# Kernel optimization log

Hardware: AMD Instinct MI355X
Metric: run time of the kernel (lower is better)

The kernel has to match this reference:

```python
import jax, jax.numpy as jnp
import numpy as np

EPS = 1e-5
K = 5

def _bn(x, g, b):
    # BatchNorm1d in training mode: biased batch statistics
    mu = jnp.mean(x, axis=0)
    var = jnp.mean((x - mu) ** 2, axis=0)
    return (x - mu) * jax.lax.rsqrt(var + EPS) * g + b

def setup_inputs():
    key = jax.random.key(0)
    ks = jax.random.split(key, 16)
    N, M, D, F = 16384, 8192, 512, 2048
    s = 0.02
    return dict(
        src=jax.random.normal(ks[0], (N, D), jnp.float32),
        anchor_2=jax.random.normal(ks[1], (M, D), jnp.float32),
        W_dim=jax.random.normal(ks[2], (D, D), jnp.float32) * s,
        b_dim=jnp.zeros((D,), jnp.float32),
        W_fus=jax.random.normal(ks[3], (2 * D, D), jnp.float32) * s,
        b_fus=jnp.zeros((D,), jnp.float32),
        W_e1=jax.random.normal(ks[4], (D, F), jnp.float32) * s,
        b_e1=jnp.zeros((F,), jnp.float32),
        W_e2=jax.random.normal(ks[5], (F, D), jnp.float32) * s,
        b_e2=jnp.zeros((D,), jnp.float32),
        g1=jnp.ones((D,), jnp.float32), bt1=jnp.zeros((D,), jnp.float32),
        g2=jnp.ones((D,), jnp.float32), bt2=jnp.zeros((D,), jnp.float32),
        W_d=jax.random.normal(ks[6], (D, D), jnp.float32) * s,
        b_d=jnp.zeros((D,), jnp.float32),
        g_d=jnp.ones((D,), jnp.float32), bt_d=jnp.zeros((D,), jnp.float32),
    )

def reference(src, anchor_2, W_dim, b_dim, W_fus, b_fus, W_e1, b_e1, W_e2, b_e2,
              g1, bt1, g2, bt2, W_d, b_d, g_d, bt_d):
    # kNN in Euclidean metric (sklearn NearestNeighbors): squared distances suffice
    # d2[n,m] = ||src_n||^2 - 2 src_n . a_m + ||a_m||^2   -> [N, M]
    d2 = (jnp.sum(src * src, axis=1, keepdims=True)
          - 2.0 * (src @ anchor_2.T)
          + jnp.sum(anchor_2 * anchor_2, axis=1)[None, :])
    _, idx = jax.lax.top_k(-d2, K)                      # [N, K] nearest anchors
    neigh = jnp.mean(anchor_2[idx], axis=1)             # gather + mean -> [N, D]
    a_map = neigh @ W_dim + b_dim                       # linear_dim
    comb = jnp.concatenate([src, a_map], axis=1) @ W_fus + b_fus
    comb = _bn(comb, g1, bt1)                           # norm1
    # encoder MLP (dropout is identity in eval)
    t = jnp.tanh(comb @ W_e1 + b_e1) @ W_e2 + b_e2
    comb = _bn(comb + t, g2, bt2)                       # residual + norm2
    out = jnp.tanh(_bn(comb @ W_d + b_d, g_d, bt_d))    # decoder
    return out
```

## Files before the change

kernel.cpp:

```cpp
#include <hip/hip_runtime.h>
#include <math.h>

#define N_ROWS 16384
#define M_ANCH 8192
#define DDIM   512
#define FDIM   2048
#define KNN    5
#define BN_EPS 1e-5f
#define CHUNK  8192
#define SEED   1024
#define CAND_MAX 256
#define MARGIN 6.0f
#define QSCALE 28.0f
#define TWO_INV_S2 (2.0f / (QSCALE * QSCALE))

typedef _Float16 f16;
typedef _Float16 f16x8 __attribute__((ext_vector_type(8)));
typedef _Float16 f16x4 __attribute__((ext_vector_type(4)));
typedef float f32x4 __attribute__((ext_vector_type(4)));
typedef int   i32x4 __attribute__((ext_vector_type(4)));

__device__ __forceinline__ void async_copy16(const void* g, void* l) {
    __builtin_amdgcn_global_load_lds(
        (const __attribute__((address_space(1))) void*)g,
        (__attribute__((address_space(3))) void*)l, 16, 0, 0);
}

__device__ __forceinline__ bool kless(float k1, int i1, float k2, int i2) {
    return (k1 < k2) || (k1 == k2 && i1 < i2);
}

__device__ __forceinline__ void insert5(float (&bk)[KNN], int (&bi)[KNN], float key, int id) {
    if (!kless(key, id, bk[4], bi[4])) return;
    bool c3 = kless(key, id, bk[3], bi[3]);
    bool c2 = kless(key, id, bk[2], bi[2]);
    bool c1 = kless(key, id, bk[1], bi[1]);
    bool c0 = kless(key, id, bk[0], bi[0]);
    bk[4] = c3 ? bk[3] : key;                  bi[4] = c3 ? bi[3] : id;
    bk[3] = c3 ? (c2 ? bk[2] : key) : bk[3];   bi[3] = c3 ? (c2 ? bi[2] : id) : bi[3];
    bk[2] = c2 ? (c1 ? bk[1] : key) : bk[2];   bi[2] = c2 ? (c1 ? bi[1] : id) : bi[2];
    bk[1] = c1 ? (c0 ? bk[0] : key) : bk[1];   bi[1] = c1 ? (c0 ? bi[0] : id) : bi[1];
    bk[0] = c0 ? key : bk[0];                  bi[0] = c0 ? id : bi[0];
}

__global__ void zero_kernel(float* p, int n) {
    int i = blockIdx.x * blockDim.x + threadIdx.x;
    if (i < n) p[i] = 0.f;
}

__global__ __launch_bounds__(256) void quant_i8_kernel(const float* __restrict__ X,
                                                       unsigned int* __restrict__ Y, int n4) {
    int i = blockIdx.x * 256 + threadIdx.x;
    if (i >= n4) return;
    float4 v = ((const float4*)X)[i];
    int a = (int)rintf(v.x * QSCALE); a = a > 127 ? 127 : (a < -127 ? -127 : a);
    int b = (int)rintf(v.y * QSCALE); b = b > 127 ? 127 : (b < -127 ? -127 : b);
    int c = (int)rintf(v.z * QSCALE); c = c > 127 ? 127 : (c < -127 ? -127 : c);
    int d = (int)rintf(v.w * QSCALE); d = d > 127 ? 127 : (d < -127 ? -127 : d);
    Y[i] = (unsigned int)(a & 255) | ((unsigned int)(b & 255) << 8)
         | ((unsigned int)(c & 255) << 16) | ((unsigned int)(d & 255) << 24);
}

__global__ __launch_bounds__(256) void rowsplit_kernel(const float* __restrict__ X,
                                                       f16* __restrict__ Y,
                                                       int n4, int log_k4) {
    int i4 = blockIdx.x * 256 + threadIdx.x;
    if (i4 >= n4) return;
    int K4 = 1 << log_k4;
    int row = i4 >> log_k4;
    int kc = (i4 & (K4 - 1)) * 4;
    float4 v = ((const float4*)X)[i4];
    f16x4 h, lo;
    h.x = (f16)v.x; h.y = (f16)v.y; h.z = (f16)v.z; h.w = (f16)v.w;
    lo.x = (f16)(v.x - (float)h.x); lo.y = (f16)(v.y - (float)h.y);
    lo.z = (f16)(v.z - (float)h.z); lo.w = (f16)(v.w - (float)h.w);
    f16* base = Y + (size_t)row * (K4 * 8) + kc;
    *(f16x4*)base = h;
    *(f16x4*)(base + K4 * 4) = lo;
}

__global__ __launch_bounds__(256) void anchor_norm_kernel(const float* __restrict__ a,
                                                          float* __restrict__ norm_a) {
    int wave = threadIdx.x >> 6, lane = threadIdx.x & 63;
    int row = blockIdx.x * 4 + wave;
    const float4* ar = (const float4*)(a + (size_t)row * DDIM);
    float4 v1 = ar[lane * 2];
    float4 v2 = ar[lane * 2 + 1];
    float s = v1.x*v1.x + v1.y*v1.y + v1.z*v1.z + v1.w*v1.w
            + v2.x*v2.x + v2.y*v2.y + v2.z*v2.z + v2.w*v2.w;
    for (int off = 32; off; off >>= 1) s += __shfl_xor(s, off, 64);
    if (lane == 0) norm_a[row] = s;
}

template<int COLLECT>
__global__ __launch_bounds__(256) void gemm_i8(
    const char* __restrict__ A, const char* __restrict__ B,
    const float* __restrict__ norm, const float* __restrict__ thr,
    int* __restrict__ cnt, int* __restrict__ cand_i, float* __restrict__ cand_n,
    int idofs, float* __restrict__ C, int Ncols)
{
    __shared__ char As[2][128 * 64];
    __shared__ char Bs[2][128 * 64];
    const int t = threadIdx.x;
    const int w = t >> 6, l = t & 63;
    const int m0 = blockIdx.y * 128, n0 = blockIdx.x * 128;
    const int wm = (w & 1) * 64, wn = (w >> 1) * 64;

    i32x4 acc[4][4];
    #pragma unroll
    for (int i = 0; i < 4; ++i)
        #pragma unroll
        for (int j = 0; j < 4; ++j) acc[i][j] = (i32x4){0, 0, 0, 0};

    const int srow = l >> 2;
    const int gq = ((l & 3) - (srow >> 1)) & 3;
    const int skoff = gq * 16;
    const int sqf = (((l >> 4) + (((l & 15) >> 1) & 3)) & 3) * 16;

    auto STAGE = [&](int buf, int kt) {
        int k0 = kt * 64;
        #pragma unroll
        for (int s = 0; s < 2; ++s) {
            int grp = w * 2 + s;
            int row = grp * 16 + srow;
            async_copy16(A + (size_t)(m0 + row) * DDIM + k0 + skoff,
                         &As[buf][grp * 1024 + l * 16]);
            async_copy16(B + (size_t)(n0 + row) * DDIM + k0 + skoff,
                         &Bs[buf][grp * 1024 + l * 16]);
        }
    };

    STAGE(0, 0);
    __syncthreads();

    for (int kt = 0; kt < 8; ++kt) {
        int cur = kt & 1;
        if (kt < 7) STAGE(cur ^ 1, kt + 1);
        i32x4 af[4], bf[4];
        #pragma unroll
        for (int i = 0; i < 4; ++i)
            af[i] = *(const i32x4*)&As[cur][(wm + i * 16 + (l & 15)) * 64 + sqf];
        #pragma unroll
        for (int j = 0; j < 4; ++j)
            bf[j] = *(const i32x4*)&Bs[cur][(wn + j * 16 + (l & 15)) * 64 + sqf];
        #pragma unroll
        for (int i = 0; i < 4; ++i)
            #pragma unroll
            for (int j = 0; j < 4; ++j)
                acc[i][j] = __builtin_amdgcn_mfma_i32_16x16x64_i8(af[i], bf[j], acc[i][j], 0, 0, 0);
        __syncthreads();
    }

    float nj[4];
    #pragma unroll
    for (int j = 0; j < 4; ++j) nj[j] = norm[n0 + wn + j * 16 + (l & 15)];

    if (COLLECT) {
        float thr4[4][4];
        #pragma unroll
        for (int i = 0; i < 4; ++i) {
            float4 tv = *(const float4*)&thr[m0 + wm + i * 16 + (l >> 4) * 4];
            thr4[i][0] = tv.x; thr4[i][1] = tv.y; thr4[i][2] = tv.z; thr4[i][3] = tv.w;
        }
        #pragma unroll
        for (int i = 0; i < 4; ++i)
            #pragma unroll
            for (int j = 0; j < 4; ++j)
                #pragma unroll
                for (int r = 0; r < 4; ++r) {
                    float key = nj[j] - TWO_INV_S2 * (float)acc[i][j][r];
                    if (key < thr4[i][r]) {
                        int row = m0 + wm + i * 16 + (l >> 4) * 4 + r;
                        int pos = atomicAdd(&cnt[row], 1);
                        if (pos < CAND_MAX) {
                            cand_i[(size_t)row * CAND_MAX + pos] =
                                idofs + n0 + wn + j * 16 + (l & 15);
                            cand_n[(size_t)row * CAND_MAX + pos] = nj[j];
                        }
                    }
                }
    } else {
        #pragma unroll
        for (int i = 0; i < 4; ++i)
            #pragma unroll
            for (int j = 0; j < 4; ++j)
                #pragma unroll
                for (int r = 0; r < 4; ++r) {
                    int m = m0 + wm + i * 16 + (l >> 4) * 4 + r;
                    int n = n0 + wn + j * 16 + (l & 15);
                    C[(size_t)m * Ncols + n] = nj[j] - TWO_INV_S2 * (float)acc[i][j][r];
                }
    }
}

__global__ __launch_bounds__(256) void topk_scan_kernel(
    const float* __restrict__ g, const float* __restrict__ norm_a,
    float* __restrict__ thrbuf, int* __restrict__ cnt,
    int* __restrict__ cand_i, float* __restrict__ cand_n)
{
    int row = blockIdx.x * 4 + (threadIdx.x >> 6);
    int lane = threadIdx.x & 63;
    const float* grow = g + (size_t)row * SEED;
    float4 v0 = *(const float4*)(grow + lane * 4);
    float4 v1 = *(const float4*)(grow + 256 + lane * 4);
    float4 v2 = *(const float4*)(grow + 512 + lane * 4);
    float4 v3 = *(const float4*)(grow + 768 + lane * 4);
    float bk[KNN]; int bi[KNN];
    #pragma unroll
    for (int q = 0; q < KNN; ++q) { bk[q] = 3.0e38f; bi[q] = 0x7fffffff; }
    int c = lane * 4;
    insert5(bk, bi, v0.x, c);       insert5(bk, bi, v0.y, c + 1);
    insert5(bk, bi, v0.z, c + 2);   insert5(bk, bi, v0.w, c + 3);
    insert5(bk, bi, v1.x, c + 256); insert5(bk, bi, v1.y, c + 257);
    insert5(bk, bi, v1.z, c + 258); insert5(bk, bi, v1.w, c + 259);
    insert5(bk, bi, v2.x, c + 512); insert5(bk, bi, v2.y, c + 513);
    insert5(bk, bi, v2.z, c + 514); insert5(bk, bi, v2.w, c + 515);
    insert5(bk, bi, v3.x, c + 768); insert5(bk, bi, v3.y, c + 769);
    insert5(bk, bi, v3.z, c + 770); insert5(bk, bi, v3.w, c + 771);
    for (int off = 32; off >= 1; off >>= 1) {
        float ok[KNN]; int oi[KNN];
        #pragma unroll
        for (int q = 0; q < KNN; ++q) {
            ok[q] = __shfl_xor(bk[q], off, 64);
            oi[q] = __shfl_xor(bi[q], off, 64);
        }
        #pragma unroll
        for (int q = 0; q < KNN; ++q) insert5(bk, bi, ok[q], oi[q]);
    }
    float thr = bk[4] + MARGIN;
    if (lane == 0) thrbuf[row] = thr;
    int* rci = cand_i + (size_t)row * CAND_MAX;
    float* rcn = cand_n + (size_t)row * CAND_MAX;
    #define PUSH(v, id) if ((v) < thr) { int pos = atomicAdd(&cnt[row], 1); \
                                         if (pos < CAND_MAX) { rci[pos] = (id); \
                                         rcn[pos] = norm_a[(id)]; } }
    PUSH(v0.x, c)       PUSH(v0.y, c + 1)   PUSH(v0.z, c + 2)   PUSH(v0.w, c + 3)
    PUSH(v1.x, c + 256) PUSH(v1.y, c + 257) PUSH(v1.z, c + 258) PUSH(v1.w, c + 259)
    PUSH(v2.x, c + 512) PUSH(v2.y, c + 513) PUSH(v2.z, c + 514) PUSH(v2.w, c + 515)
    PUSH(v3.x, c + 768) PUSH(v3.y, c + 769) PUSH(v3.z, c + 770) PUSH(v3.w, c + 771)
    #undef PUSH
}

__global__ __launch_bounds__(256) void rescore_kernel(
    const float* __restrict__ src, const float* __restrict__ anchor,
    const int* __restrict__ cnt, const int* __restrict__ cand_i,
    const float* __restrict__ cand_n, float* __restrict__ neigh)
{
    __shared__ float lb[4][2][DDIM];
    int wv = threadIdx.x >> 6, lane = threadIdx.x & 63;
    int row = blockIdx.x * 4 + wv;
    const float4* sp = (const float4*)(src + (size_t)row * DDIM);
    float4 s0 = sp[lane * 2], s1 = sp[lane * 2 + 1];
    int c = cnt[row]; if (c > CAND_MAX) c = CAND_MAX;
    const int* ci = cand_i + (size_t)row * CAND_MAX;
    const float* cn = cand_n + (size_t)row * CAND_MAX;

    float bk[KNN]; int bi[KNN];
    #pragma unroll
    for (int q = 0; q < KNN; ++q) { bk[q] = 3.0e38f; bi[q] = 0x7fffffff; }

    auto PREF = [&](int buf, int id) {
        const float* gp = anchor + (size_t)id * DDIM;
        async_copy16(gp + lane * 8,     &lb[wv][buf][lane * 4]);
        async_copy16(gp + lane * 8 + 4, &lb[wv][buf][256 + lane * 4]);
    };

    int   id_c = ci[0];          float n_c = cn[0];
    int   id_n = ci[1];          float n_n = cn[1];
    PREF(0, id_c);
    PREF(1, id_n);

    for (int p = 0; p < c; ++p) {
        int id_f = 0; float n_f = 0.f;
        if (p + 2 < c) { id_f = ci[p + 2]; n_f = cn[p + 2]; }
        asm volatile("s_waitcnt vmcnt(4)" ::: "memory");
        const float* bc = &lb[wv][p & 1][0];
        float4 a0 = *(const float4*)&bc[lane * 4];
        float4 a1 = *(const float4*)&bc[256 + lane * 4];
        float d = s0.x*a0.x + s0.y*a0.y + s0.z*a0.z + s0.w*a0.w
                + s1.x*a1.x + s1.y*a1.y + s1.z*a1.z + s1.w*a1.w;
        #pragma unroll
        for (int off = 32; off; off >>= 1) d += __shfl_xor(d, off, 64);
        insert5(bk, bi, n_c - 2.f * d, id_c);
        if (p + 2 < c) PREF(p & 1, id_f);
        id_c = id_n; n_c = n_n;
        id_n = id_f; n_n = n_f;
    }

    const float4* a0 = (const float4*)(anchor + (size_t)bi[0] * DDIM);
    const float4* a1 = (const float4*)(anchor + (size_t)bi[1] * DDIM);
    const float4* a2 = (const float4*)(anchor + (size_t)bi[2] * DDIM);
    const float4* a3 = (const float4*)(anchor + (size_t)bi[3] * DDIM);
    const float4* a4 = (const float4*)(anchor + (size_t)bi[4] * DDIM);
    float4* np = (float4*)(neigh + (size_t)row * DDIM);
    #pragma unroll
    for (int p = 0; p < 2; ++p) {
        int c4 = lane + 64 * p;
        float4 v0 = a0[c4], v1 = a1[c4], v2 = a2[c4], v3 = a3[c4], v4 = a4[c4];
        float4 o;
        o.x = (v0.x + v1.x + v2.x + v3.x + v4.x) * 0.2f;
        o.y = (v0.y + v1.y + v2.y + v3.y + v4.y) * 0.2f;
        o.z = (v0.z + v1.z + v2.z + v3.z + v4.z) * 0.2f;
        o.w = (v0.w + v1.w + v2.w + v3.w + v4.w) * 0.2f;
        np[c4] = o;
    }
}

template<int ADDC0, int TANH, int K>
__global__ __launch_bounds__(256) void gemm_f16hl(
    const f16* __restrict__ Aw, const f16* __restrict__ Bw,
    const float* __restrict__ bias, const float* __restrict__ C0,
    float* __restrict__ C, int Ncols)
{
    __shared__ f16 Ah[2][128 * 32];
    __shared__ f16 Al[2][128 * 32];
    __shared__ f16 Bh[2][128 * 32];
    __shared__ f16 Bl[2][128 * 32];
    const int t = threadIdx.x;
    const int w = t >> 6, l = t & 63;
    const int m0 = blockIdx.y * 128, n0 = blockIdx.x * 128;
    const int wm = (w & 1) * 64, wn = (w >> 1) * 64;
    const int K2 = 2 * K;
    const int NK = K / 32;

    f32x4 acc[4][4];
    #pragma unroll
    for (int i = 0; i < 4; ++i)
        #pragma unroll
        for (int j = 0; j < 4; ++j) acc[i][j] = (f32x4){0.f, 0.f, 0.f, 0.f};

    const int srow = l >> 2;
    const int gq = ((l & 3) - (srow >> 1)) & 3;
    const int skoff = gq * 8;
    const int sqf = (((l >> 4) + (((l & 15) >> 1) & 3)) & 3) * 8;

    auto STAGE = [&](int buf, int kt) {
        int k0 = kt * 32;
        #pragma unroll
        for (int s = 0; s < 2; ++s) {
            int grp = w * 2 + s;
            int row = grp * 16 + srow;
            const f16* ap = Aw + (size_t)(m0 + row) * K2 + k0 + skoff;
            async_copy16(ap,     &Ah[buf][grp * 512 + l * 8]);
            async_copy16(ap + K, &Al[buf][grp * 512 + l * 8]);
            const f16* bp = Bw + (size_t)(n0 + row) * K2 + k0 + skoff;
            async_copy16(bp,     &Bh[buf][grp * 512 + l * 8]);
            async_copy16(bp + K, &Bl[buf][grp * 512 + l * 8]);
        }
    };

    STAGE(0, 0);
    __syncthreads();

    for (int kt = 0; kt < NK; ++kt) {
        int cur = kt & 1;
        if (kt + 1 < NK) STAGE(cur ^ 1, kt + 1);
        f16x8 afh[4], afl[4], bfh[4], bfl[4];
        #pragma unroll
        for (int i = 0; i < 4; ++i) {
            int base = (wm + i * 16 + (l & 15)) * 32 + sqf;
            afh[i] = *(const f16x8*)&Ah[cur][base];
            afl[i] = *(const f16x8*)&Al[cur][base];
        }
        #pragma unroll
        for (int j = 0; j < 4; ++j) {
            int base = (wn + j * 16 + (l & 15)) * 32 + sqf;
            bfh[j] = *(const f16x8*)&Bh[cur][base];
            bfl[j] = *(const f16x8*)&Bl[cur][base];
        }
        #pragma unroll
        for (int i = 0; i < 4; ++i)
            #pragma unroll
            for (int j = 0; j < 4; ++j) {
                acc[i][j] = __builtin_amdgcn_mfma_f32_16x16x32_f16(afh[i], bfh[j], acc[i][j], 0, 0, 0);
                acc[i][j] = __builtin_amdgcn_mfma_f32_16x16x32_f16(afl[i], bfh[j], acc[i][j], 0, 0, 0);
                acc[i][j] = __builtin_amdgcn_mfma_f32_16x16x32_f16(afh[i], bfl[j], acc[i][j], 0, 0, 0);
            }
        __syncthreads();
    }
    float bv[4];
    #pragma unroll
    for (int j = 0; j < 4; ++j)
        bv[j] = bias ? bias[n0 + wn + j * 16 + (l & 15)] : 0.f;
    #pragma unroll
    for (int i = 0; i < 4; ++i)
        #pragma unroll
        for (int j = 0; j < 4; ++j)
            #pragma unroll
            for (int r = 0; r < 4; ++r) {
                int m = m0 + wm + i * 16 + (l >> 4) * 4 + r;
                int n = n0 + wn + j * 16 + (l & 15);
                float v = acc[i][j][r] + bv[j];
                if (ADDC0) v += C0[(size_t)m * Ncols + n];
                if (TANH)  v = tanhf(v);
                C[(size_t)m * Ncols + n] = v;
            }
}

__global__ __launch_bounds__(256) void wsplit_kernel(const float* __restrict__ W,
                                                     f16* __restrict__ Wt,
                                                     int K, int N)
{
    __shared__ float tile[64][65];
    const int t = threadIdx.x;
    const int kb = blockIdx.y * 64, nb = blockIdx.x * 64;
    #pragma unroll
    for (int i = 0; i < 4; ++i) {
        int r = (t >> 4) + i * 16;
        int c = (t & 15) * 4;
        *(float4*)&tile[r][c] = *(const float4*)&W[(size_t)(kb + r) * N + nb + c];
    }
    __syncthreads();
    const int r2 = t >> 2;
    const int kc = (t & 3) * 16;
    f16x8 h0, h1, lo0, lo1;
    #pragma unroll
    for (int e = 0; e < 8; ++e) {
        float x = tile[kc + e][r2];
        f16 hh = (f16)x; h0[e] = hh; lo0[e] = (f16)(x - (float)hh);
        float y = tile[kc + 8 + e][r2];
        f16 hh2 = (f16)y; h1[e] = hh2; lo1[e] = (f16)(y - (float)hh2);
    }
    f16* base = Wt + (size_t)(nb + r2) * 2 * K + kb + kc;
    *(f16x8*)base = h0; *(f16x8*)(base + 8) = h1;
    *(f16x8*)(base + K) = lo0; *(f16x8*)(base + K + 8) = lo1;
}

__global__ __launch_bounds__(256) void bcomb_kernel(const float* __restrict__ b_dim,
                                                    const float* __restrict__ W_fus2,
                                                    const float* __restrict__ b_fus,
                                                    float* __restrict__ b_comb)
{
    int n = blockIdx.x * 256 + threadIdx.x;
    if (n >= DDIM) return;
    float s = b_fus[n];
    for (int k = 0; k < DDIM; ++k) s += b_dim[k] * W_fus2[(size_t)k * DDIM + n];
    b_comb[n] = s;
}

template<int ACT>
__global__ __launch_bounds__(256) void gemm_kernel(
    const float* __restrict__ A, int K1,
    const float* __restrict__ A2, int K2,
    const float* __restrict__ B, const float* __restrict__ bias,
    float* __restrict__ C, int Ncols)
{
    __shared__ float As[16][132];
    __shared__ float Bs[16][128];
    const int t = threadIdx.x;
    const int n0 = blockIdx.x * 128;
    const int m0 = blockIdx.y * 128;
    const int ty = t >> 4, tx = t & 15;
    const int K = K1 + K2;

    float acc[8][8];
    #pragma unroll
    for (int i = 0; i < 8; ++i)
        #pragma unroll
        for (int j = 0; j < 8; ++j) acc[i][j] = 0.f;

    const int ar = t >> 1;
    const int akc = (t & 1) * 8;
    const int bkr = t >> 4;
    const int bc = (t & 15) * 8;

    for (int k0 = 0; k0 < K; k0 += 16) {
        int kk = k0 + akc;
        float4 v0, v1;
        if (kk < K1) {
            const float* p = A + (size_t)(m0 + ar) * K1 + kk;
            v0 = *(const float4*)p; v1 = *(const float4*)(p + 4);
        } else {
            const float* p = A2 + (size_t)(m0 + ar) * K2 + (kk - K1);
            v0 = *(const float4*)p; v1 = *(const float4*)(p + 4);
        }
        const float* bp = B + (size_t)(k0 + bkr) * Ncols + n0 + bc;
        float4 w0 = *(const float4*)bp, w1 = *(const float4*)(bp + 4);
        __syncthreads();
        As[akc+0][ar] = v0.x; As[akc+1][ar] = v0.y; As[akc+2][ar] = v0.z; As[akc+3][ar] = v0.w;
        As[akc+4][ar] = v1.x; As[akc+5][ar] = v1.y; As[akc+6][ar] = v1.z; As[akc+7][ar] = v1.w;
        *(float4*)&Bs[bkr][bc] = w0; *(float4*)&Bs[bkr][bc + 4] = w1;
        __syncthreads();
        #pragma unroll
        for (int k = 0; k < 16; ++k) {
            float a[8], b[8];
            *(float4*)&a[0] = *(const float4*)&As[k][ty * 8];
            *(float4*)&a[4] = *(const float4*)&As[k][ty * 8 + 4];
            *(float4*)&b[0] = *(const float4*)&Bs[k][tx * 4];
            *(float4*)&b[4] = *(const float4*)&Bs[k][64 + tx * 4];
            #pragma unroll
            for (int i = 0; i < 8; ++i)
                #pragma unroll
                for (int j = 0; j < 8; ++j) acc[i][j] += a[i] * b[j];
        }
    }
    float4 bv0 = *(const float4*)(bias + n0 + tx * 4);
    float4 bv1 = *(const float4*)(bias + n0 + 64 + tx * 4);
    #pragma unroll
    for (int i = 0; i < 8; ++i) {
        int row = m0 + ty * 8 + i;
        float4 o0, o1;
        o0.x = acc[i][0] + bv0.x; o0.y = acc[i][1] + bv0.y;
        o0.z = acc[i][2] + bv0.z; o0.w = acc[i][3] + bv0.w;
        o1.x = acc[i][4] + bv1.x; o1.y = acc[i][5] + bv1.y;
        o1.z = acc[i][6] + bv1.z; o1.w = acc[i][7] + bv1.w;
        if (ACT == 1) {
            o0.x = tanhf(o0.x); o0.y = tanhf(o0.y); o0.z = tanhf(o0.z); o0.w = tanhf(o0.w);
            o1.x = tanhf(o1.x); o1.y = tanhf(o1.y); o1.z = tanhf(o1.z); o1.w = tanhf(o1.w);
        }
        *(float4*)(C + (size_t)row * Ncols + n0 + tx * 4) = o0;
        *(float4*)(C + (size_t)row * Ncols + n0 + 64 + tx * 4) = o1;
    }
}

__global__ __launch_bounds__(256) void bn_stats_kernel(const float* __restrict__ X,
                                                       float* __restrict__ sums)
{
    __shared__ float red[8][64];
    int lane = threadIdx.x & 63;
    int rl = threadIdx.x >> 6;
    int c = blockIdx.x * 64 + lane;
    int chunk = N_ROWS / gridDim.y;
    int rbeg = blockIdx.y * chunk;
    float s = 0.f, s2 = 0.f;
    for (int r = rbeg + rl; r < rbeg + chunk; r += 4) {
        float v = X[(size_t)r * DDIM + c];
        s += v; s2 += v * v;
    }
    red[rl][lane] = s; red[4 + rl][lane] = s2;
    __syncthreads();
    if (threadIdx.x < 64) {
        float ts = red[0][lane] + red[1][lane] + red[2][lane] + red[3][lane];
        float t2 = red[4][lane] + red[5][lane] + red[6][lane] + red[7][lane];
        atomicAdd(&sums[c], ts);
        atomicAdd(&sums[DDIM + c], t2);
    }
}

template<int TANH>
__global__ __launch_bounds__(256) void bn_apply_kernel(
    const float* __restrict__ X, float* __restrict__ Y,
    const float* __restrict__ sums, const float* __restrict__ g,
    const float* __restrict__ b, float invN)
{
    size_t i = (size_t)blockIdx.x * 256 + threadIdx.x;
    int cg = (int)(i % (DDIM / 4));
    int c = cg * 4;
    float4 x = ((const float4*)X)[i];
    float4 sm = *(const float4*)(sums + c);
    float4 sq = *(const float4*)(sums + DDIM + c);
    float4 gv = *(const float4*)(g + c);
    float4 bv = *(const float4*)(b + c);
    float m, var, rs;
    m = sm.x * invN; var = sq.x * invN - m * m; rs = rsqrtf(var + BN_EPS);
    x.x = (x.x - m) * rs * gv.x + bv.x;
    m = sm.y * invN; var = sq.y * invN - m * m; rs = rsqrtf(var + BN_EPS);
    x.y = (x.y - m) * rs * gv.y + bv.y;
    m = sm.z * invN; var = sq.z * invN - m * m; rs = rsqrtf(var + BN_EPS);
    x.z = (x.z - m) * rs * gv.z + bv.z;
    m = sm.w * invN; var = sq.w * invN - m * m; rs = rsqrtf(var + BN_EPS);
    x.w = (x.w - m) * rs * gv.w + bv.w;
    if (TANH) { x.x = tanhf(x.x); x.y = tanhf(x.y); x.z = tanhf(x.z); x.w = tanhf(x.w); }
    ((float4*)Y)[i] = x;
}

extern "C" void kernel_launch(void* const* d_in, const int* in_sizes, int n_in,
                              void* d_out, int out_size, void* d_ws, size_t ws_size,
                              hipStream_t stream)
{
    const float* src   = (const float*)d_in[0];
    const float* anc   = (const float*)d_in[1];
    const float* W_dim = (const float*)d_in[2];
    const float* b_dim = (const float*)d_in[3];
    const float* W_fus = (const float*)d_in[4];
    const float* b_fus = (const float*)d_in[5];
    const float* W_e1  = (const float*)d_in[6];
    const float* b_e1  = (const float*)d_in[7];
    const float* W_e2  = (const float*)d_in[8];
    const float* b_e2  = (const float*)d_in[9];
    const float* g1    = (const float*)d_in[10];
    const float* bt1   = (const float*)d_in[11];
    const float* g2    = (const float*)d_in[12];
    const float* bt2   = (const float*)d_in[13];
    const float* W_d   = (const float*)d_in[14];
    const float* b_d   = (const float*)d_in[15];
    const float* g_d   = (const float*)d_in[16];
    const float* bt_d  = (const float*)d_in[17];
    float* out = (float*)d_out;

    float* ws = (float*)d_ws;
    float* score  = ws;
    float* bufA   = ws + 16777216;
    char*  src2q  = (char*)(ws + 25165824);
    char*  anc2q  = (char*)(ws + 37748736);
    f16*   wbase  = (f16*)(ws + 25165824);
    f16*   Wt_fus1  = wbase;
    f16*   Wt_comb2 = wbase + 524288;
    f16*   Wt_e1    = wbase + 1048576;
    f16*   Wt_e2    = wbase + 3145728;
    f16*   Wt_d     = wbase + 5242880;
    f16*   aslot    = (f16*)(ws + 28049408);
    f16*   h_h      = (f16*)(ws + 28049408);
    f16*   combh    = (f16*)(ws + 44826624);
    float* cand_n   = ws + 29360128;
    float* W_comb2  = ws + 44040192;
    float* norm_a   = ws + 44302336;
    float* thrbuf   = ws + 44478464;
    int*   cnt      = (int*)(ws + 44494848);
    int*   cand_i   = (int*)(ws + 48705536);
    float* sums1    = ws + 49020928;
    float* sums2    = sums1 + 1024;
    float* sums3    = sums2 + 1024;
    float* zeros512 = ws + 49024000;
    float* b_comb   = ws + 49024512;

    const float invN = 1.0f / (float)N_ROWS;
    float* hbuf = score;

    zero_kernel<<<dim3(64), 256, 0, stream>>>((float*)cnt, 16384);
    quant_i8_kernel<<<dim3(N_ROWS * DDIM / 1024), 256, 0, stream>>>(
        src, (unsigned int*)src2q, N_ROWS * DDIM / 4);
    quant_i8_kernel<<<dim3(M_ANCH * DDIM / 1024), 256, 0, stream>>>(
        anc, (unsigned int*)anc2q, M_ANCH * DDIM / 4);
    anchor_norm_kernel<<<dim3(M_ANCH / 4), 256, 0, stream>>>(anc, norm_a);

    gemm_i8<0><<<dim3(SEED / 128, N_ROWS / 128), 256, 0, stream>>>(
        src2q, anc2q, norm_a, nullptr, nullptr, nullptr, nullptr, 0, score, SEED);
    topk_scan_kernel<<<dim3(N_ROWS / 4), 256, 0, stream>>>(
        score, norm_a, thrbuf, cnt, cand_i, cand_n);
    gemm_i8<1><<<dim3((M_ANCH - SEED) / 128, N_ROWS / 128), 256, 0, stream>>>(
        src2q, anc2q + (size_t)SEED * DDIM, norm_a + SEED, thrbuf,
        cnt, cand_i, cand_n, SEED, nullptr, 0);
    rescore_kernel<<<dim3(N_ROWS / 4), 256, 0, stream>>>(
        src, anc, cnt, cand_i, cand_n, bufA);

    zero_kernel<<<dim3(14), 256, 0, stream>>>(sums1, 3584);

    wsplit_kernel<<<dim3(DDIM / 64, DDIM / 64), 256, 0, stream>>>(W_fus, Wt_fus1, DDIM, DDIM);
    wsplit_kernel<<<dim3(FDIM / 64, DDIM / 64), 256, 0, stream>>>(W_e1, Wt_e1, DDIM, FDIM);
    wsplit_kernel<<<dim3(DDIM / 64, FDIM / 64), 256, 0, stream>>>(W_e2, Wt_e2, FDIM, DDIM);
    wsplit_kernel<<<dim3(DDIM / 64, DDIM / 64), 256, 0, stream>>>(W_d, Wt_d, DDIM, DDIM);
    gemm_kernel<0><<<dim3(4, 4), 256, 0, stream>>>(
        W_dim, DDIM, nullptr, 0, W_fus + DDIM * DDIM, zeros512, W_comb2, DDIM);
    bcomb_kernel<<<dim3(2), 256, 0, stream>>>(b_dim, W_fus + DDIM * DDIM, b_fus, b_comb);
    wsplit_kernel<<<dim3(DDIM / 64, DDIM / 64), 256, 0, stream>>>(W_comb2, Wt_comb2, DDIM, DDIM);

    rowsplit_kernel<<<dim3(N_ROWS * DDIM / 1024), 256, 0, stream>>>(
        src, aslot, N_ROWS * DDIM / 4, 7);
    gemm_f16hl<0, 0, DDIM><<<dim3(DDIM / 128, N_ROWS / 128), 256, 0, stream>>>(
        aslot, Wt_fus1, b_comb, nullptr, out, DDIM);
    rowsplit_kernel<<<dim3(N_ROWS * DDIM / 1024), 256, 0, stream>>>(
        bufA, aslot, N_ROWS * DDIM / 4, 7);
    gemm_f16hl<1, 0, DDIM><<<dim3(DDIM / 128, N_ROWS / 128), 256, 0, stream>>>(
        aslot, Wt_comb2, nullptr, out, out, DDIM);
    bn_stats_kernel<<<dim3(DDIM / 64, 16), 256, 0, stream>>>(out, sums1);
    bn_apply_kernel<0><<<dim3(8192), 256, 0, stream>>>(out, out, sums1, g1, bt1, invN);

    for (int r0 = 0; r0 < N_ROWS; r0 += CHUNK) {
        rowsplit_kernel<<<dim3(CHUNK * DDIM / 1024), 256, 0, stream>>>(
            out + (size_t)r0 * DDIM, combh, CHUNK * DDIM / 4, 7);
        gemm_f16hl<0, 1, DDIM><<<dim3(FDIM / 128, CHUNK / 128), 256, 0, stream>>>(
            combh, Wt_e1, b_e1, nullptr, hbuf, FDIM);
        rowsplit_kernel<<<dim3(CHUNK * FDIM / 1024), 256, 0, stream>>>(
            hbuf, h_h, CHUNK * FDIM / 4, 9);
        gemm_f16hl<1, 0, FDIM><<<dim3(DDIM / 128, CHUNK / 128), 256, 0, stream>>>(
            h_h, Wt_e2, b_e2, out + (size_t)r0 * DDIM, bufA + (size_t)r0 * DDIM,
            DDIM);
    }
    bn_stats_kernel<<<dim3(DDIM / 64, 16), 256, 0, stream>>>(bufA, sums2);
    bn_apply_kernel<0><<<dim3(8192), 256, 0, stream>>>(bufA, bufA, sums2, g2, bt2, invN);

    rowsplit_kernel<<<dim3(N_ROWS * DDIM / 1024), 256, 0, stream>>>(
        bufA, aslot, N_ROWS * DDIM / 4, 7);
    gemm_f16hl<0, 0, DDIM><<<dim3(DDIM / 128, N_ROWS / 128), 256, 0, stream>>>(
        aslot, Wt_d, b_d, nullptr, out, DDIM);
    bn_stats_kernel<<<dim3(DDIM / 64, 16), 256, 0, stream>>>(out, sums3);
    bn_apply_kernel<1><<<dim3(8192), 256, 0, stream>>>(out, out, sums3, g_d, bt_d, invN);
}
```

Measured before the change: 1.711 ms.

## Drop activation low-half split, fuse f16 casts into epilogues, unchunk encoder MLP

```diff
diff --git a/kernel.cpp b/kernel.cpp
--- a/kernel.cpp
+++ b/kernel.cpp
@@ -7,7 +7,6 @@
 #define FDIM   2048
 #define KNN    5
 #define BN_EPS 1e-5f
-#define CHUNK  8192
 #define SEED   1024
 #define CAND_MAX 256
 #define MARGIN 6.0f
@@ -61,22 +60,14 @@
          | ((unsigned int)(c & 255) << 16) | ((unsigned int)(d & 255) << 24);
 }
 
-__global__ __launch_bounds__(256) void rowsplit_kernel(const float* __restrict__ X,
-                                                       f16* __restrict__ Y,
-                                                       int n4, int log_k4) {
-    int i4 = blockIdx.x * 256 + threadIdx.x;
-    if (i4 >= n4) return;
-    int K4 = 1 << log_k4;
-    int row = i4 >> log_k4;
-    int kc = (i4 & (K4 - 1)) * 4;
-    float4 v = ((const float4*)X)[i4];
-    f16x4 h, lo;
+__global__ __launch_bounds__(256) void cast_f16_kernel(const float* __restrict__ X,
+                                                       f16* __restrict__ Y, int n4) {
+    int i = blockIdx.x * 256 + threadIdx.x;
+    if (i >= n4) return;
+    float4 v = ((const float4*)X)[i];
+    f16x4 h;
     h.x = (f16)v.x; h.y = (f16)v.y; h.z = (f16)v.z; h.w = (f16)v.w;
-    lo.x = (f16)(v.x - (float)h.x); lo.y = (f16)(v.y - (float)h.y);
-    lo.z = (f16)(v.z - (float)h.z); lo.w = (f16)(v.w - (float)h.w);
-    f16* base = Y + (size_t)row * (K4 * 8) + kc;
-    *(f16x4*)base = h;
-    *(f16x4*)(base + K4 * 4) = lo;
+    ((f16x4*)Y)[i] = h;
 }
 
 __global__ __launch_bounds__(256) void anchor_norm_kernel(const float* __restrict__ a,
@@ -306,14 +297,13 @@
     }
 }
 
-template<int ADDC0, int TANH, int K>
-__global__ __launch_bounds__(256) void gemm_f16hl(
+template<int ADDC0, int TANH, int WF16, int K>
+__global__ __launch_bounds__(256) void gemm_f16a(
     const f16* __restrict__ Aw, const f16* __restrict__ Bw,
     const float* __restrict__ bias, const float* __restrict__ C0,
-    float* __restrict__ C, int Ncols)
+    void* __restrict__ Cv, int Ncols)
 {
     __shared__ f16 Ah[2][128 * 32];
-    __shared__ f16 Al[2][128 * 32];
     __shared__ f16 Bh[2][128 * 32];
     __shared__ f16 Bl[2][128 * 32];
     const int t = threadIdx.x;
@@ -340,9 +330,8 @@
         for (int s = 0; s < 2; ++s) {
             int grp = w * 2 + s;
             int row = grp * 16 + srow;
-            const f16* ap = Aw + (size_t)(m0 + row) * K2 + k0 + skoff;
-            async_copy16(ap,     &Ah[buf][grp * 512 + l * 8]);
-            async_copy16(ap + K, &Al[buf][grp * 512 + l * 8]);
+            async_copy16(Aw + (size_t)(m0 + row) * K + k0 + skoff,
+                         &Ah[buf][grp * 512 + l * 8]);
             const f16* bp = Bw + (size_t)(n0 + row) * K2 + k0 + skoff;
             async_copy16(bp,     &Bh[buf][grp * 512 + l * 8]);
             async_copy16(bp + K, &Bl[buf][grp * 512 + l * 8]);
@@ -355,13 +344,10 @@
     for (int kt = 0; kt < NK; ++kt) {
         int cur = kt & 1;
         if (kt + 1 < NK) STAGE(cur ^ 1, kt + 1);
-        f16x8 afh[4], afl[4], bfh[4], bfl[4];
-        #pragma unroll
-        for (int i = 0; i < 4; ++i) {
-            int base = (wm + i * 16 + (l & 15)) * 32 + sqf;
-            afh[i] = *(const f16x8*)&Ah[cur][base];
-            afl[i] = *(const f16x8*)&Al[cur][base];
-        }
+        f16x8 af[4], bfh[4], bfl[4];
+        #pragma unroll
+        for (int i = 0; i < 4; ++i)
+            af[i] = *(const f16x8*)&Ah[cur][(wm + i * 16 + (l & 15)) * 32 + sqf];
         #pragma unroll
         for (int j = 0; j < 4; ++j) {
             int base = (wn + j * 16 + (l & 15)) * 32 + sqf;
@@ -372,9 +358,8 @@
         for (int i = 0; i < 4; ++i)
             #pragma unroll
             for (int j = 0; j < 4; ++j) {
-                acc[i][j] = __builtin_amdgcn_mfma_f32_16x16x32_f16(afh[i], bfh[j], acc[i][j], 0, 0, 0);
-                acc[i][j] = __builtin_amdgcn_mfma_f32_16x16x32_f16(afl[i], bfh[j], acc[i][j], 0, 0, 0);
-                acc[i][j] = __builtin_amdgcn_mfma_f32_16x16x32_f16(afh[i], bfl[j], acc[i][j], 0, 0, 0);
+                acc[i][j] = __builtin_amdgcn_mfma_f32_16x16x32_f16(af[i], bfh[j], acc[i][j], 0, 0, 0);
+                acc[i][j] = __builtin_amdgcn_mfma_f32_16x16x32_f16(af[i], bfl[j], acc[i][j], 0, 0, 0);
             }
         __syncthreads();
     }
@@ -393,7 +378,8 @@
                 float v = acc[i][j][r] + bv[j];
                 if (ADDC0) v += C0[(size_t)m * Ncols + n];
                 if (TANH)  v = tanhf(v);
-                C[(size_t)m * Ncols + n] = v;
+                if (WF16)  ((f16*)Cv)[(size_t)m * Ncols + n] = (f16)v;
+                else       ((float*)Cv)[(size_t)m * Ncols + n] = v;
             }
 }
 
@@ -539,7 +525,7 @@
 
 template<int TANH>
 __global__ __launch_bounds__(256) void bn_apply_kernel(
-    const float* __restrict__ X, float* __restrict__ Y,
+    const float* __restrict__ X, float* __restrict__ Y, f16* __restrict__ Yh,
     const float* __restrict__ sums, const float* __restrict__ g,
     const float* __restrict__ b, float invN)
 {
@@ -562,6 +548,11 @@
     x.w = (x.w - m) * rs * gv.w + bv.w;
     if (TANH) { x.x = tanhf(x.x); x.y = tanhf(x.y); x.z = tanhf(x.z); x.w = tanhf(x.w); }
     ((float4*)Y)[i] = x;
+    if (Yh) {
+        f16x4 h;
+        h.x = (f16)x.x; h.y = (f16)x.y; h.z = (f16)x.z; h.w = (f16)x.w;
+        ((f16x4*)Yh)[i] = h;
+    }
 }
 
 extern "C" void kernel_launch(void* const* d_in, const int* in_sizes, int n_in,
@@ -599,9 +590,10 @@
     f16*   Wt_e1    = wbase + 1048576;
     f16*   Wt_e2    = wbase + 3145728;
     f16*   Wt_d     = wbase + 5242880;
-    f16*   aslot    = (f16*)(ws + 28049408);
-    f16*   h_h      = (f16*)(ws + 28049408);
-    f16*   combh    = (f16*)(ws + 44826624);
+    f16*   hH       = (f16*)ws;
+    f16*   srcH     = (f16*)(ws + 28049408);
+    f16*   aH       = (f16*)(ws + 32243712);
+    f16*   combH    = (f16*)(ws + 36438016);
     float* cand_n   = ws + 29360128;
     float* W_comb2  = ws + 44040192;
     float* norm_a   = ws + 44302336;
@@ -615,7 +607,6 @@
     float* b_comb   = ws + 49024512;
 
     const float invN = 1.0f / (float)N_ROWS;
-    float* hbuf = score;
 
     zero_kernel<<<dim3(64), 256, 0, stream>>>((float*)cnt, 16384);
     quant_i8_kernel<<<dim3(N_ROWS * DDIM / 1024), 256, 0, stream>>>(
@@ -645,35 +636,26 @@
     bcomb_kernel<<<dim3(2), 256, 0, stream>>>(b_dim, W_fus + DDIM * DDIM, b_fus, b_comb);
     wsplit_kernel<<<dim3(DDIM / 64, DDIM / 64), 256, 0, stream>>>(W_comb2, Wt_comb2, DDIM, DDIM);
 
-    rowsplit_kernel<<<dim3(N_ROWS * DDIM / 1024), 256, 0, stream>>>(
-        src, aslot, N_ROWS * DDIM / 4, 7);
-    gemm_f16hl<0, 0, DDIM><<<dim3(DDIM / 128, N_ROWS / 128), 256, 0, stream>>>(
-        aslot, Wt_fus1, b_comb, nullptr, out, DDIM);
-    rowsplit_kernel<<<dim3(N_ROWS * DDIM / 1024), 256, 0, stream>>>(
-        bufA, aslot, N_ROWS * DDIM / 4, 7);
-    gemm_f16hl<1, 0, DDIM><<<dim3(DDIM / 128, N_ROWS / 128), 256, 0, stream>>>(
-        aslot, Wt_comb2, nullptr, out, out, DDIM);
+    cast_f16_kernel<<<dim3(N_ROWS * DDIM / 1024), 256, 0, stream>>>(
+        src, srcH, N_ROWS * DDIM / 4);
+    gemm_f16a<0, 0, 0, DDIM><<<dim3(DDIM / 128, N_ROWS / 128), 256, 0, stream>>>(
+        srcH, Wt_fus1, b_comb, nullptr, out, DDIM);
+    cast_f16_kernel<<<dim3(N_ROWS * DDIM / 1024), 256, 0, stream>>>(
+        bufA, aH, N_ROWS * DDIM / 4);
+    gemm_f16a<1, 0, 0, DDIM><<<dim3(DDIM / 128, N_ROWS / 128), 256, 0, stream>>>(
+        aH, Wt_comb2, nullptr, out, out, DDIM);
     bn_stats_kernel<<<dim3(DDIM / 64, 16), 256, 0, stream>>>(out, sums1);
-    bn_apply_kernel<0><<<dim3(8192), 256, 0, stream>>>(out, out, sums1, g1, bt1, invN);
-
-    for (int r0 = 0; r0 < N_ROWS; r0 += CHUNK) {
-        rowsplit_kernel<<<dim3(CHUNK * DDIM / 1024), 256, 0, stream>>>(
-            out + (size_t)r0 * DDIM, combh, CHUNK * DDIM / 4, 7);
-        gemm_f16hl<0, 1, DDIM><<<dim3(FDIM / 128, CHUNK / 128), 256, 0, stream>>>(
-            combh, Wt_e1, b_e1, nullptr, hbuf, FDIM);
-        rowsplit_kernel<<<dim3(CHUNK * FDIM / 1024), 256, 0, stream>>>(
-            hbuf, h_h, CHUNK * FDIM / 4, 9);
-        gemm_f16hl<1, 0, FDIM><<<dim3(DDIM / 128, CHUNK / 128), 256, 0, stream>>>(
-            h_h, Wt_e2, b_e2, out + (size_t)r0 * DDIM, bufA + (size_t)r0 * DDIM,
-            DDIM);
-    }
+    bn_apply_kernel<0><<<dim3(8192), 256, 0, stream>>>(out, out, combH, sums1, g1, bt1, invN);
+
+    gemm_f16a<0, 1, 1, DDIM><<<dim3(FDIM / 128, N_ROWS / 128), 256, 0, stream>>>(
+        combH, Wt_e1, b_e1, nullptr, hH, FDIM);
+    gemm_f16a<1, 0, 0, FDIM><<<dim3(DDIM / 128, N_ROWS / 128), 256, 0, stream>>>(
+        hH, Wt_e2, b_e2, out, bufA, DDIM);
     bn_stats_kernel<<<dim3(DDIM / 64, 16), 256, 0, stream>>>(bufA, sums2);
-    bn_apply_kernel<0><<<dim3(8192), 256, 0, stream>>>(bufA, bufA, sums2, g2, bt2, invN);
-
-    rowsplit_kernel<<<dim3(N_ROWS * DDIM / 1024), 256, 0, stream>>>(
-        bufA, aslot, N_ROWS * DDIM / 4, 7);
-    gemm_f16hl<0, 0, DDIM><<<dim3(DDIM / 128, N_ROWS / 128), 256, 0, stream>>>(
-        aslot, Wt_d, b_d, nullptr, out, DDIM);
+    bn_apply_kernel<0><<<dim3(8192), 256, 0, stream>>>(bufA, bufA, aH, sums2, g2, bt2, invN);
+
+    gemm_f16a<0, 0, 0, DDIM><<<dim3(DDIM / 128, N_ROWS / 128), 256, 0, stream>>>(
+        aH, Wt_d, b_d, nullptr, out, DDIM);
     bn_stats_kernel<<<dim3(DDIM / 64, 16), 256, 0, stream>>>(out, sums3);
-    bn_apply_kernel<1><<<dim3(8192), 256, 0, stream>>>(out, out, sums3, g_d, bt_d, invN);
-}
+    bn_apply_kernel<1><<<dim3(8192), 256, 0, stream>>>(out, out, nullptr, sums3, g_d, bt_d, invN);
+}
```

After: 1.396 ms. 18.4% less time.
